# Optimization experiments

Measured on AMD Instinct MI355X. Metric: run time of the kernel, lower is better.

The kernel has to match this reference:

```python
import jax, jax.numpy as jnp
import numpy as np

D_MODEL = 1024
N_HEADS = 16
D_HEAD = D_MODEL // N_HEADS
B, S = 2, 2048


def setup_inputs() -> dict:
    key = jax.random.key(0)
    ks = jax.random.split(key, 8)
    scale = 1.0 / np.sqrt(D_MODEL)
    return {
        "x": jax.random.normal(ks[0], (B, S, D_MODEL), dtype=jnp.float32),
        "Wq": jax.random.normal(ks[1], (D_MODEL, D_MODEL), dtype=jnp.float32) * scale,
        "bq": jnp.zeros((D_MODEL,), dtype=jnp.float32),
        "Wk": jax.random.normal(ks[2], (D_MODEL, D_MODEL), dtype=jnp.float32) * scale,
        "bk": jnp.zeros((D_MODEL,), dtype=jnp.float32),
        "Wv": jax.random.normal(ks[3], (D_MODEL, D_MODEL), dtype=jnp.float32) * scale,
        "bv": jnp.zeros((D_MODEL,), dtype=jnp.float32),
        "Wo": jax.random.normal(ks[4], (D_MODEL, D_MODEL), dtype=jnp.float32) * scale,
    }


def reference(x, Wq, bq, Wk, bk, Wv, bv, Wo):
    Bsz, Slen, D = x.shape
    # projections -> [B, H, S, Dh]
    def split_heads(t):
        return t.reshape(Bsz, Slen, N_HEADS, D_HEAD).transpose(0, 2, 1, 3)
    q = split_heads(x @ Wq + bq)
    k = split_heads(x @ Wk + bk)
    v = split_heads(x @ Wv + bv)
    scale = jnp.sqrt(jnp.float32(D_HEAD))
    scores = jnp.einsum('bhsd,bhtd->bhst', q, k) / scale  # [B,H,S,S]
    causal_mask = jnp.tril(jnp.ones((Slen, Slen), dtype=jnp.bool_))
    scores = jnp.where(causal_mask, scores, jnp.finfo(scores.dtype).min)
    attn = jax.nn.softmax(scores, axis=-1)
    # deterministic=True path: dropout is identity
    out = jnp.einsum('bhst,bhtd->bhsd', attn, v)
    out = out.transpose(0, 2, 1, 3).reshape(Bsz, Slen, D)
    return out @ Wo
```

## Files before the change

kernel.cpp:

```cpp
#include <hip/hip_runtime.h>
#include <hip/hip_bf16.h>

#define BATCH   2
#define SEQ     2048
#define DMODEL  1024
#define NHEADS  16
#define DHEAD   64
#define MROWS   (BATCH*SEQ)
#define NBH     (BATCH*NHEADS)

typedef float  f32x4  __attribute__((ext_vector_type(4)));
typedef short  s16x4  __attribute__((ext_vector_type(4)));
typedef short  s16x8  __attribute__((ext_vector_type(8)));
typedef __bf16 bf16x8 __attribute__((ext_vector_type(8)));

__device__ __forceinline__ short f2bf(float f) {
  union { float f; unsigned u; } v; v.f = f;
  return (short)((v.u + 0x7fffu + ((v.u >> 16) & 1u)) >> 16);
}
__device__ __forceinline__ float bf2f(short s) {
  union { unsigned u; float f; } v; v.u = ((unsigned)(unsigned short)s) << 16;
  return v.f;
}

__global__ void convert_x(const float* __restrict__ x, short* __restrict__ xb) {
  int i = (blockIdx.x * 256 + threadIdx.x) * 4;
  float4 v = *(const float4*)(x + i);
  s16x4 o = { f2bf(v.x), f2bf(v.y), f2bf(v.z), f2bf(v.w) };
  *(s16x4*)(xb + i) = o;
}

__global__ void transpose_w(const float* __restrict__ Wq, const float* __restrict__ Wk,
                            const float* __restrict__ Wv, const float* __restrict__ Wo,
                            short* __restrict__ WtQKV, short* __restrict__ WtO) {
  __shared__ float t[32][33];
  const float* W; short* Wt;
  int z = blockIdx.z;
  if      (z == 0) { W = Wq; Wt = WtQKV; }
  else if (z == 1) { W = Wk; Wt = WtQKV + (1u << 20); }
  else if (z == 2) { W = Wv; Wt = WtQKV + (2u << 20); }
  else             { W = Wo; Wt = WtO; }
  int n0 = blockIdx.x * 32, k0 = blockIdx.y * 32;
  int tx = threadIdx.x, ty = threadIdx.y;
  #pragma unroll
  for (int i = 0; i < 32; i += 8) t[ty + i][tx] = W[(k0 + ty + i) * DMODEL + n0 + tx];
  __syncthreads();
  #pragma unroll
  for (int i = 0; i < 32; i += 8) Wt[(n0 + ty + i) * DMODEL + k0 + tx] = f2bf(t[tx][ty + i]);
}

template<int MT, int NT, int EPI>
__global__ __launch_bounds__(256) void gemm_bf16(
    const short* __restrict__ A, const short* __restrict__ Bt,
    const float* __restrict__ bq, const float* __restrict__ bk, const float* __restrict__ bv,
    short* __restrict__ qb, short* __restrict__ kb, short* __restrict__ vt,
    float* __restrict__ out)
{
  constexpr int K = DMODEL, BK = 32;
  constexpr int WM = MT / 2, WN = NT / 2;
  constexpr int TM = WM / 16, TN = WN / 16;
  constexpr int CA = MT * BK / 512;
  constexpr int CB = NT * BK / 512;
  constexpr int TP = 136;
  constexpr int SME = (EPI == 0) ? 128 * TP : (MT * BK + NT * BK);
  __shared__ short smem[SME];
  short* la = smem;
  short* lb = smem + MT * BK;
  const int tid = threadIdx.x;
  const int wave = tid >> 6, lane = tid & 63;
  const int quad = lane >> 4, l16 = lane & 15;
  const int wr = wave >> 1, wc = wave & 1;
  const int m0 = blockIdx.y * MT, n0 = blockIdx.x * NT;
  const int arow = lane >> 2, acol = (lane & 3) * 8;

  f32x4 acc[TM][TN] = {};

  for (int k0 = 0; k0 < K; k0 += BK) {
    for (int c = wave; c < CA; c += 4) {
      const short* gp = A + (m0 + c * 16 + arow) * K + k0 + acol;
      __builtin_amdgcn_global_load_lds((__attribute__((address_space(1))) void*)gp,
                                       (__attribute__((address_space(3))) void*)(la + c * 512),
                                       16, 0, 0);
    }
    for (int c = wave; c < CB; c += 4) {
      const short* gp = Bt + (n0 + c * 16 + arow) * K + k0 + acol;
      __builtin_amdgcn_global_load_lds((__attribute__((address_space(1))) void*)gp,
                                       (__attribute__((address_space(3))) void*)(lb + c * 512),
                                       16, 0, 0);
    }
    __syncthreads();
    bf16x8 af[TM], bfr[TN];
    #pragma unroll
    for (int i = 0; i < TM; ++i)
      af[i] = *(const bf16x8*)&la[(wr * WM + i * 16 + l16) * BK + quad * 8];
    #pragma unroll
    for (int j = 0; j < TN; ++j)
      bfr[j] = *(const bf16x8*)&lb[(wc * WN + j * 16 + l16) * BK + quad * 8];
    #pragma unroll
    for (int i = 0; i < TM; ++i)
      #pragma unroll
      for (int j = 0; j < TN; ++j)
        acc[i][j] = __builtin_amdgcn_mfma_f32_16x16x32_bf16(af[i], bfr[j], acc[i][j], 0, 0, 0);
    __syncthreads();
  }

  if constexpr (EPI == 0) {
    const bool isV = (n0 >= 2 * DMODEL);
    const float* bias; int nbase; float scl;
    if (n0 < DMODEL)          { bias = bq; nbase = 0;          scl = 0.125f * 1.44269504089f; }
    else if (n0 < 2 * DMODEL) { bias = bk; nbase = DMODEL;     scl = 1.f; }
    else                      { bias = bv; nbase = 2 * DMODEL; scl = 1.f; }
    #pragma unroll
    for (int j = 0; j < TN; ++j) {
      int coll = wc * WN + j * 16 + l16;
      float bias_v = bias[n0 - nbase + coll];
      #pragma unroll
      for (int i = 0; i < TM; ++i) {
        int rowl = wr * WM + i * 16 + quad * 4;
        #pragma unroll
        for (int r = 0; r < 4; ++r) {
          short v = f2bf((acc[i][j][r] + bias_v) * scl);
          if (isV) smem[coll * TP + rowl + r] = v;
          else     smem[(rowl + r) * TP + coll] = v;
        }
      }
    }
    __syncthreads();
    const int b = m0 >> 11, s0 = m0 & (SEQ - 1);
    const int rseg = tid & 15, rrow = tid >> 4;
    if (!isV) {
      short* dst = (n0 < DMODEL) ? qb : kb;
      #pragma unroll
      for (int it = 0; it < 8; ++it) {
        int row = it * 16 + rrow;
        int colg = (n0 - nbase) + rseg * 8;
        int h = colg >> 6, d = colg & 63;
        s16x8 v = *(const s16x8*)&smem[row * TP + rseg * 8];
        *(s16x8*)(dst + ((b * NHEADS + h) * SEQ + s0 + row) * DHEAD + d) = v;
      }
    } else {
      #pragma unroll
      for (int it = 0; it < 8; ++it) {
        int drow = it * 16 + rrow;
        int colg = (n0 - nbase) + drow;
        int h = colg >> 6, d = colg & 63;
        s16x8 v = *(const s16x8*)&smem[drow * TP + rseg * 8];
        *(s16x8*)(vt + ((b * NHEADS + h) * DHEAD + d) * SEQ + s0 + rseg * 8) = v;
      }
    }
  } else {
    #pragma unroll
    for (int i = 0; i < TM; ++i)
      #pragma unroll
      for (int r = 0; r < 4; ++r) {
        int mrow = m0 + wr * WM + i * 16 + quad * 4 + r;
        #pragma unroll
        for (int j = 0; j < TN; ++j)
          out[mrow * DMODEL + n0 + wc * WN + j * 16 + l16] = acc[i][j][r];
      }
    (void)bq; (void)bk; (void)bv; (void)qb; (void)kb; (void)vt;
  }
}


__global__ __launch_bounds__(256, 2) void attn_k(
    const short* __restrict__ qbp, const short* __restrict__ kbp,
    const short* __restrict__ vtb, short* __restrict__ oP, float* __restrict__ lP)
{
  __shared__ short kls[2][4096];
  __shared__ short vls[2][4096];
  const int tid = threadIdx.x, wave = tid >> 6, lane = tid & 63;
  const int quad = lane >> 4, l16 = lane & 15;
  const int half = blockIdx.x & 1;
  const int bh = (blockIdx.x >> 1) & 31;
  const int qg = blockIdx.x >> 6;
  const int qt1 = qg * 8 + wave * 2;
  const int mF[4] = { qt1 * 16, (qt1 + 1) * 16, (126 - qt1) * 16, (127 - qt1) * 16 };
  const int nch = (127 - 8 * qg) / 4 + 1;
  const short* Q  = qbp + bh * SEQ * DHEAD;
  const short* Kp = kbp + bh * SEQ * DHEAD;
  const short* Vt = vtb + bh * DHEAD * SEQ;

  bf16x8 qf[4][2];
  #pragma unroll
  for (int f = 0; f < 4; ++f) {
    qf[f][0] = *(const bf16x8*)&Q[(mF[f] + l16) * DHEAD + quad * 8];
    qf[f][1] = *(const bf16x8*)&Q[(mF[f] + l16) * DHEAD + 32 + quad * 8];
  }

  float lF[4] = {};
  f32x4 oF[4][4] = {};

  const int vdl = lane >> 3, vsl = lane & 7;

  auto stage = [&](int buf, int t0) {
    #pragma unroll
    for (int j = 0; j < 2; ++j) {
      int g = j * 4 + wave;
      const short* gp = Kp + (t0 + lane) * DHEAD + g * 8;
      __builtin_amdgcn_global_load_lds((__attribute__((address_space(1))) void*)gp,
                                       (__attribute__((address_space(3))) void*)&kls[buf][g * 512],
                                       16, 0, 0);
    }
    #pragma unroll
    for (int j = 0; j < 2; ++j) {
      int gd = j * 4 + wave;
      const short* gp = Vt + (gd * 8 + vdl) * SEQ + t0 + ((vsl ^ vdl) * 8);
      __builtin_amdgcn_global_load_lds((__attribute__((address_space(1))) void*)gp,
                                       (__attribute__((address_space(3))) void*)&vls[buf][gd * 512],
                                       16, 0, 0);
    }
  };

  stage(0, half * 64);
  for (int c = half; c < nch; c += 2) {
    __syncthreads();
    if (c + 2 < nch) stage(((c >> 1) + 1) & 1, (c + 2) * 64);
    const int t0 = c * 64;
    const int buf = (c >> 1) & 1;
    #pragma unroll
    for (int t = 0; t < 4; ++t) {
      const int tb = t0 + t * 16;
      if (tb <= mF[3]) {
        bf16x8 kf0 = *(const bf16x8*)&kls[buf][((0 + quad) * 64 + t * 16 + l16) * 8];
        bf16x8 kf1 = *(const bf16x8*)&kls[buf][((4 + quad) * 64 + t * 16 + l16) * 8];
        s16x4 vf[4];
        {
          int gsw = ((t * 2 + (quad >> 1)) ^ (l16 & 7));
          #pragma unroll
          for (int dt = 0; dt < 4; ++dt)
            vf[dt] = *(const s16x4*)&vls[buf][((dt * 16 + l16) * 8 + gsw) * 8 + (quad & 1) * 4];
        }
        #pragma unroll
        for (int f = 0; f < 4; ++f) {
          if (tb <= mF[f]) {
            f32x4 a = {};
            a = __builtin_amdgcn_mfma_f32_16x16x32_bf16(kf0, qf[f][0], a, 0, 0, 0);
            a = __builtin_amdgcn_mfma_f32_16x16x32_bf16(kf1, qf[f][1], a, 0, 0, 0);
            if (tb == mF[f]) {
              #pragma unroll
              for (int r = 0; r < 4; ++r)
                if (quad * 4 + r > l16) a[r] = -1e30f;
            }
            f32x4 p;
            #pragma unroll
            for (int r = 0; r < 4; ++r) p[r] = __builtin_amdgcn_exp2f(a[r]);
            lF[f] += (p[0] + p[1]) + (p[2] + p[3]);
            __hip_bfloat162 c01 = __float22bfloat162_rn(float2{p[0], p[1]});
            __hip_bfloat162 c23 = __float22bfloat162_rn(float2{p[2], p[3]});
            union { unsigned u[2]; s16x4 s; } pu;
            pu.u[0] = *(unsigned*)&c01; pu.u[1] = *(unsigned*)&c23;
            #pragma unroll
            for (int dt = 0; dt < 4; ++dt)
              oF[f][dt] = __builtin_amdgcn_mfma_f32_16x16x16bf16_1k(pu.s, vf[dt], oF[f][dt], 0, 0, 0);
          }
        }
      }
    }
  }

  float* lD = lP + (half * NBH + bh) * SEQ;
  short* oD = oP + ((half * NBH + bh) * SEQ) * DHEAD;
  #pragma unroll
  for (int f = 0; f < 4; ++f) {
    float l = lF[f];
    l += __shfl_xor(l, 16, 64); l += __shfl_xor(l, 32, 64);
    if (quad == 0) lD[mF[f] + l16] = l;
    #pragma unroll
    for (int r = 0; r < 4; ++r) {
      int s = mF[f] + quad * 4 + r;
      #pragma unroll
      for (int dt = 0; dt < 4; ++dt)
        oD[s * DHEAD + dt * 16 + l16] = f2bf(oF[f][dt][r]);
    }
  }
}

__global__ void attn_merge(const short* __restrict__ oP, const float* __restrict__ lP,
                           short* __restrict__ ob) {
  int idx = blockIdx.x * 256 + threadIdx.x;
  int d8 = idx & 7, s = (idx >> 3) & (SEQ - 1), bh = idx >> 14;
  s16x8 e = *(const s16x8*)&oP[((0   + bh) * SEQ + s) * DHEAD + d8 * 8];
  s16x8 o = *(const s16x8*)&oP[((NBH + bh) * SEQ + s) * DHEAD + d8 * 8];
  float linv = 1.0f / (lP[bh * SEQ + s] + lP[(NBH + bh) * SEQ + s]);
  s16x8 r;
  #pragma unroll
  for (int k = 0; k < 8; ++k) r[k] = f2bf((bf2f(e[k]) + bf2f(o[k])) * linv);
  int b = bh >> 4, h = bh & 15;
  *(s16x8*)&ob[(b * SEQ + s) * DMODEL + h * DHEAD + d8 * 8] = r;
}

extern "C" void kernel_launch(void* const* d_in, const int* in_sizes, int n_in,
                              void* d_out, int out_size, void* d_ws, size_t ws_size,
                              hipStream_t stream) {
  const float* x  = (const float*)d_in[0];
  const float* Wq = (const float*)d_in[1];
  const float* bq = (const float*)d_in[2];
  const float* Wk = (const float*)d_in[3];
  const float* bk = (const float*)d_in[4];
  const float* Wv = (const float*)d_in[5];
  const float* bv = (const float*)d_in[6];
  const float* Wo = (const float*)d_in[7];
  float* out = (float*)d_out;

  char* ws = (char*)d_ws;
  short* xb  = (short*)(ws);
  short* wtq = (short*)(ws + (8u  << 20));
  short* oP  = (short*)(ws);
  short* qb  = (short*)(ws + (16u << 20));
  short* kb  = (short*)(ws + (24u << 20));
  short* vt  = (short*)(ws + (32u << 20));
  short* ob  = (short*)(ws + (40u << 20));
  short* wto = (short*)(ws + (48u << 20));
  float* lP  = (float*)(ws + (50u << 20));

  convert_x<<<MROWS * DMODEL / 1024, 256, 0, stream>>>(x, xb);
  transpose_w<<<dim3(32, 32, 4), dim3(32, 8), 0, stream>>>(Wq, Wk, Wv, Wo, wtq, wto);

  gemm_bf16<128, 128, 0><<<dim3(3 * DMODEL / 128, MROWS / 128), 256, 0, stream>>>(
      xb, wtq, bq, bk, bv, qb, kb, vt, nullptr);

  attn_k<<<NBH * 8 * 2, 256, 0, stream>>>(qb, kb, vt, oP, lP);
  attn_merge<<<NBH * SEQ * 8 / 256, 256, 0, stream>>>(oP, lP, ob);

  gemm_bf16<64, 128, 1><<<dim3(DMODEL / 128, MROWS / 64), 256, 0, stream>>>(
      ob, wto, nullptr, nullptr, nullptr, nullptr, nullptr, nullptr, out);
}
```

Measured before the change: 192.9 us.

## Split attention KV range four ways and fuse input prep kernels

The attention kernel now splits each query group's key range across four blocks instead of two, which doubles the grid and raises the occupancy hint to 4 blocks per CU. The merge kernel sums four partial outputs and row sums. The x conversion and weight transposes are combined into one launch, and the workspace layout is moved so the larger partial buffers fit. The aim is better CU utilisation and one less launch, at the cost of more partial-output traffic in the merge and more register pressure from the tighter launch bound.

```diff
diff --git a/kernel.cpp b/kernel.cpp
--- a/kernel.cpp
+++ b/kernel.cpp
@@ -23,25 +23,27 @@
   return v.f;
 }
 
-__global__ void convert_x(const float* __restrict__ x, short* __restrict__ xb) {
-  int i = (blockIdx.x * 256 + threadIdx.x) * 4;
-  float4 v = *(const float4*)(x + i);
-  s16x4 o = { f2bf(v.x), f2bf(v.y), f2bf(v.z), f2bf(v.w) };
-  *(s16x4*)(xb + i) = o;
-}
-
-__global__ void transpose_w(const float* __restrict__ Wq, const float* __restrict__ Wk,
-                            const float* __restrict__ Wv, const float* __restrict__ Wo,
-                            short* __restrict__ WtQKV, short* __restrict__ WtO) {
+__global__ void prep_fused(const float* __restrict__ x, short* __restrict__ xb,
+                           const float* __restrict__ Wq, const float* __restrict__ Wk,
+                           const float* __restrict__ Wv, const float* __restrict__ Wo,
+                           short* __restrict__ WtQKV, short* __restrict__ WtO) {
   __shared__ float t[32][33];
+  int z = blockIdx.z;
+  int tx = threadIdx.x, ty = threadIdx.y;
+  if (z >= 4) {
+    int blk = (z - 4) * 1024 + blockIdx.y * 32 + blockIdx.x;
+    int i = (blk * 256 + ty * 32 + tx) * 4;
+    float4 v = *(const float4*)(x + i);
+    s16x4 o = { f2bf(v.x), f2bf(v.y), f2bf(v.z), f2bf(v.w) };
+    *(s16x4*)(xb + i) = o;
+    return;
+  }
   const float* W; short* Wt;
-  int z = blockIdx.z;
   if      (z == 0) { W = Wq; Wt = WtQKV; }
   else if (z == 1) { W = Wk; Wt = WtQKV + (1u << 20); }
   else if (z == 2) { W = Wv; Wt = WtQKV + (2u << 20); }
   else             { W = Wo; Wt = WtO; }
   int n0 = blockIdx.x * 32, k0 = blockIdx.y * 32;
-  int tx = threadIdx.x, ty = threadIdx.y;
   #pragma unroll
   for (int i = 0; i < 32; i += 8) t[ty + i][tx] = W[(k0 + ty + i) * DMODEL + n0 + tx];
   __syncthreads();
@@ -163,7 +165,7 @@
 }
 
 
-__global__ __launch_bounds__(256, 2) void attn_k(
+__global__ __launch_bounds__(256, 4) void attn_k(
     const short* __restrict__ qbp, const short* __restrict__ kbp,
     const short* __restrict__ vtb, short* __restrict__ oP, float* __restrict__ lP)
 {
@@ -171,9 +173,9 @@
   __shared__ short vls[2][4096];
   const int tid = threadIdx.x, wave = tid >> 6, lane = tid & 63;
   const int quad = lane >> 4, l16 = lane & 15;
-  const int half = blockIdx.x & 1;
-  const int bh = (blockIdx.x >> 1) & 31;
-  const int qg = blockIdx.x >> 6;
+  const int qtr = blockIdx.x & 3;
+  const int bh = (blockIdx.x >> 2) & 31;
+  const int qg = blockIdx.x >> 7;
   const int qt1 = qg * 8 + wave * 2;
   const int mF[4] = { qt1 * 16, (qt1 + 1) * 16, (126 - qt1) * 16, (127 - qt1) * 16 };
   const int nch = (127 - 8 * qg) / 4 + 1;
@@ -212,12 +214,12 @@
     }
   };
 
-  stage(0, half * 64);
-  for (int c = half; c < nch; c += 2) {
+  stage(0, qtr * 64);
+  for (int c = qtr; c < nch; c += 4) {
     __syncthreads();
-    if (c + 2 < nch) stage(((c >> 1) + 1) & 1, (c + 2) * 64);
+    if (c + 4 < nch) stage(((c >> 2) + 1) & 1, (c + 4) * 64);
     const int t0 = c * 64;
-    const int buf = (c >> 1) & 1;
+    const int buf = (c >> 2) & 1;
     #pragma unroll
     for (int t = 0; t < 4; ++t) {
       const int tb = t0 + t * 16;
@@ -259,8 +261,8 @@
     }
   }
 
-  float* lD = lP + (half * NBH + bh) * SEQ;
-  short* oD = oP + ((half * NBH + bh) * SEQ) * DHEAD;
+  float* lD = lP + (qtr * NBH + bh) * SEQ;
+  short* oD = oP + ((qtr * NBH + bh) * SEQ) * DHEAD;
   #pragma unroll
   for (int f = 0; f < 4; ++f) {
     float l = lF[f];
@@ -280,12 +282,19 @@
                            short* __restrict__ ob) {
   int idx = blockIdx.x * 256 + threadIdx.x;
   int d8 = idx & 7, s = (idx >> 3) & (SEQ - 1), bh = idx >> 14;
-  s16x8 e = *(const s16x8*)&oP[((0   + bh) * SEQ + s) * DHEAD + d8 * 8];
-  s16x8 o = *(const s16x8*)&oP[((NBH + bh) * SEQ + s) * DHEAD + d8 * 8];
-  float linv = 1.0f / (lP[bh * SEQ + s] + lP[(NBH + bh) * SEQ + s]);
+  float acc[8] = {};
+  float lsum = 0.f;
+  #pragma unroll
+  for (int q = 0; q < 4; ++q) {
+    s16x8 e = *(const s16x8*)&oP[((q * NBH + bh) * SEQ + s) * DHEAD + d8 * 8];
+    #pragma unroll
+    for (int k = 0; k < 8; ++k) acc[k] += bf2f(e[k]);
+    lsum += lP[(q * NBH + bh) * SEQ + s];
+  }
+  float linv = 1.0f / lsum;
   s16x8 r;
   #pragma unroll
-  for (int k = 0; k < 8; ++k) r[k] = f2bf((bf2f(e[k]) + bf2f(o[k])) * linv);
+  for (int k = 0; k < 8; ++k) r[k] = f2bf(acc[k] * linv);
   int b = bh >> 4, h = bh & 15;
   *(s16x8*)&ob[(b * SEQ + s) * DMODEL + h * DHEAD + d8 * 8] = r;
 }
@@ -306,21 +315,20 @@
   char* ws = (char*)d_ws;
   short* xb  = (short*)(ws);
   short* wtq = (short*)(ws + (8u  << 20));
-  short* oP  = (short*)(ws);
+  short* wto = (short*)(ws + (14u << 20));
   short* qb  = (short*)(ws + (16u << 20));
   short* kb  = (short*)(ws + (24u << 20));
   short* vt  = (short*)(ws + (32u << 20));
   short* ob  = (short*)(ws + (40u << 20));
-  short* wto = (short*)(ws + (48u << 20));
-  float* lP  = (float*)(ws + (50u << 20));
-
-  convert_x<<<MROWS * DMODEL / 1024, 256, 0, stream>>>(x, xb);
-  transpose_w<<<dim3(32, 32, 4), dim3(32, 8), 0, stream>>>(Wq, Wk, Wv, Wo, wtq, wto);
+  short* oP  = (short*)(ws + (48u << 20));
+  float* lP  = (float*)(ws + (80u << 20));
+
+  prep_fused<<<dim3(32, 32, 8), dim3(32, 8), 0, stream>>>(x, xb, Wq, Wk, Wv, Wo, wtq, wto);
 
   gemm_bf16<128, 128, 0><<<dim3(3 * DMODEL / 128, MROWS / 128), 256, 0, stream>>>(
       xb, wtq, bq, bk, bv, qb, kb, vt, nullptr);
 
-  attn_k<<<NBH * 8 * 2, 256, 0, stream>>>(qb, kb, vt, oP, lP);
+  attn_k<<<8 * NBH * 4, 256, 0, stream>>>(qb, kb, vt, oP, lP);
   attn_merge<<<NBH * SEQ * 8 / 256, 256, 0, stream>>>(oP, lP, ob);
 
   gemm_bf16<64, 128, 1><<<dim3(DMODEL / 128, MROWS / 64), 256, 0, stream>>>(
```

New measurement: 213.5 us. 10.7% more time.
